# Optimization experiments

Hardware: AMD Instinct MI355X
Metric: run time of the kernel (lower is better)

## Reference

```python
import jax, jax.numpy as jnp
import numpy as np

N, E, H, FN, FE = 50000, 800000, 128, 8, 4


def setup_inputs() -> dict:
    key = jax.random.key(0)
    ks = jax.random.split(key, 12)
    g = lambda k, shape: jax.random.normal(k, shape, dtype=jnp.float32) * 0.05
    return dict(
        x=jax.random.normal(ks[0], (N, FN), dtype=jnp.float32),
        edge_index=jax.random.randint(ks[1], (2, E), 0, N),
        edge_attr=jax.random.normal(ks[2], (E, FE), dtype=jnp.float32),
        W1=g(ks[3], (FN, H)), b1=jnp.zeros((H,), jnp.float32),
        W2=g(ks[4], (H, H)), b2=jnp.zeros((H,), jnp.float32),
        W3=g(ks[5], (H, H)), b3=jnp.zeros((H,), jnp.float32),
        We1=g(ks[6], (FE, H)), be1=jnp.zeros((H,), jnp.float32),
        We2=g(ks[7], (H, H)), be2=jnp.zeros((H,), jnp.float32),
        Wc1=g(ks[8], (3 * H, H)), bc1=jnp.zeros((H,), jnp.float32),
        Wc2=g(ks[9], (H, H // 2)), bc2=jnp.zeros((H // 2,), jnp.float32),
        Wc3=g(ks[10], (H // 2, 2)), bc3=jnp.zeros((2,), jnp.float32),
    )


def _gcn(h, W, b, row2, col2, norm, n):
    # GCNConv: transform, normalized message from source row2 -> target col2, scatter-add, bias
    h = h @ W
    msg = norm[:, None] * h[row2]  # [E+N, H]
    return jax.ops.segment_sum(msg, col2, num_segments=n) + b


def reference(x, edge_index, edge_attr, W1, b1, W2, b2, W3, b3,
              We1, be1, We2, be2, Wc1, bc1, Wc2, bc2, Wc3, bc3):
    n = x.shape[0]
    row, col = edge_index[0], edge_index[1]
    loop = jnp.arange(n)
    # add self-loops (PyG GCNConv default)
    row2 = jnp.concatenate([row, loop])
    col2 = jnp.concatenate([col, loop])
    deg = jax.ops.segment_sum(jnp.ones_like(col2, dtype=x.dtype), col2, num_segments=n)
    dinv = jnp.where(deg > 0, deg ** -0.5, 0.0)
    norm = dinv[row2] * dinv[col2]  # symmetric normalization per edge

    h = jax.nn.relu(_gcn(x, W1, b1, row2, col2, norm, n))
    h = jax.nn.relu(_gcn(h, W2, b2, row2, col2, norm, n))
    h = jax.nn.relu(_gcn(h, W3, b3, row2, col2, norm, n))

    # edge encoder MLP (dropout inactive in eval)
    ef = jax.nn.relu(edge_attr @ We1 + be1) @ We2 + be2

    # gather endpoint node features, concat with edge features
    ec = jnp.concatenate([h[row], h[col], ef], axis=1)  # [E, 3H]
    z = jax.nn.relu(ec @ Wc1 + bc1)
    z = jax.nn.relu(z @ Wc2 + bc2)
    logits = z @ Wc3 + bc3
    return jax.nn.log_softmax(logits, axis=1)
```

## Files before the change

### kernel.cpp

```cpp
#include <hip/hip_runtime.h>
#include <math.h>

#define H 128
#define STC 152
#define SOT 136
#define SPQ 136
#define Z2S 69

typedef __attribute__((ext_vector_type(8))) short short8;
typedef __attribute__((ext_vector_type(4))) float f32x4;

__device__ inline float bflo(unsigned int v) { return __uint_as_float(v << 16); }
__device__ inline float bfhi(unsigned int v) { return __uint_as_float(v & 0xffff0000u); }
__device__ inline float bf2f(unsigned short v) { return __uint_as_float(((unsigned int)v) << 16); }

__device__ inline unsigned int cvtpk(float lo, float hi) {
    unsigned int r;
    asm("v_cvt_pk_bf16_f32 %0, %1, %2" : "=v"(r) : "v"(lo), "v"(hi));
    return r;
}
__device__ inline unsigned short f2bf1(float f) {
    unsigned int r;
    asm("v_cvt_pk_bf16_f32 %0, %1, %1" : "=v"(r) : "v"(f));
    return (unsigned short)r;
}


__global__ void count_kernel(const int* __restrict__ col, int E, int* __restrict__ cnt) {
    int e = blockIdx.x * blockDim.x + threadIdx.x;
    if (e < E) atomicAdd(&cnt[col[e]], 1);
}

__global__ void scan_sum_kernel(const int* __restrict__ cnt, int N, int* __restrict__ bsum) {
    int b = blockIdx.x, t = threadIdx.x;
    int base = b * 1024 + t * 4;
    int s = 0;
#pragma unroll
    for (int g = 0; g < 4; ++g) {
        int i = base + g;
        if (i < N) s += cnt[i];
    }
    for (int off = 32; off >= 1; off >>= 1) s += __shfl_down(s, off, 64);
    __shared__ int ws[4];
    if ((t & 63) == 0) ws[t >> 6] = s;
    __syncthreads();
    if (t == 0) bsum[b] = ws[0] + ws[1] + ws[2] + ws[3];
}

__global__ void scan_offsets_kernel(const int* __restrict__ bsum, int nb,
                                    int* __restrict__ boff, int* __restrict__ col_start, int N) {
    int lane = threadIdx.x;
    int v = (lane < nb) ? bsum[lane] : 0;
    int incl = v;
    for (int off = 1; off < 64; off <<= 1) {
        int u = __shfl_up(incl, off, 64);
        if (lane >= off) incl += u;
    }
    if (lane < nb) boff[lane] = incl - v;
    if (lane == 63) col_start[N] = incl;
}

__global__ void scan_write_kernel(const int* __restrict__ cnt, int N, const int* __restrict__ boff,
                                  int* __restrict__ col_start, int* __restrict__ cursor,
                                  float* __restrict__ dinv) {
    int b = blockIdx.x, t = threadIdx.x;
    int lane = t & 63, wv = t >> 6;
    int base = b * 1024 + t * 4;
    int c[4];
    int s = 0;
#pragma unroll
    for (int g = 0; g < 4; ++g) {
        int i = base + g;
        c[g] = (i < N) ? cnt[i] : 0;
        s += c[g];
    }
    int incl = s;
    for (int off = 1; off < 64; off <<= 1) {
        int u = __shfl_up(incl, off, 64);
        if (lane >= off) incl += u;
    }
    __shared__ int ws[4];
    if (lane == 63) ws[wv] = incl;
    __syncthreads();
    int run = boff[b] + incl - s;
    for (int w = 0; w < wv; ++w) run += ws[w];
#pragma unroll
    for (int g = 0; g < 4; ++g) {
        int i = base + g;
        if (i < N) {
            col_start[i] = run;
            cursor[i] = run;
            dinv[i] = rsqrtf((float)(c[g] + 1));
            run += c[g];
        }
    }
}

__global__ void scatter_kernel(const int* __restrict__ row, const int* __restrict__ col, int E,
                               int* __restrict__ cursor, int* __restrict__ csc_src,
                               int2* __restrict__ csc_ec) {
    int e = blockIdx.x * blockDim.x + threadIdx.x;
    if (e < E) {
        int c = col[e];
        int p = atomicAdd(&cursor[c], 1);
        csc_src[p] = row[e];
        csc_ec[p] = make_int2(e, c);
    }
}


__global__ __launch_bounds__(256) void aggx_kernel(
    const float* __restrict__ x, const int* __restrict__ col_start,
    const int* __restrict__ csc_src, const float* __restrict__ dinv,
    float* __restrict__ aggx, int N) {
    int wv = threadIdx.x >> 6, lane = threadIdx.x & 63;
    int i = blockIdx.x * 4 + wv;
    if (i >= N) return;
    int f = lane & 7, j = lane >> 3;
    int s0 = col_start[i], s1 = col_start[i + 1];
    float acc = 0.f;
    int p = s0 + j;
    for (; p + 8 < s1; p += 16) {
        int sa = csc_src[p], sb = csc_src[p + 8];
        float va = dinv[sa] * x[sa * 8 + f];
        float vb = dinv[sb] * x[sb * 8 + f];
        acc += va + vb;
    }
    if (p < s1) {
        int s = csc_src[p];
        acc = fmaf(dinv[s], x[s * 8 + f], acc);
    }
    acc += __shfl_xor(acc, 8, 64);
    acc += __shfl_xor(acc, 16, 64);
    acc += __shfl_xor(acc, 32, 64);
    if (j == 0) {
        float di = dinv[i];
        aggx[i * 8 + f] = fmaf(di, acc, di * di * x[i * 8 + f]);
    }
}

__global__ void xform8bf_kernel(const float* __restrict__ aggx, const float* __restrict__ W,
                                const float* __restrict__ b, const float* __restrict__ dinv,
                                unsigned int* __restrict__ out, int N) {
    int t = blockIdx.x * 256 + threadIdx.x;
    int i = t >> 6, jp = t & 63;
    if (i >= N) return;
    const float* ar = aggx + i * 8;
    float sc = dinv[i];
    int j0 = jp * 2;
    float a0 = b[j0], a1 = b[j0 + 1];
#pragma unroll
    for (int k = 0; k < 8; ++k) {
        float av = ar[k];
        a0 = fmaf(av, W[k * 128 + j0], a0);
        a1 = fmaf(av, W[k * 128 + j0 + 1], a1);
    }
    out[(size_t)i * 64 + jp] = cvtpk(sc * fmaxf(a0, 0.f), sc * fmaxf(a1, 0.f));
}

__global__ __launch_bounds__(256) void agg128bf_kernel(
    const unsigned int* __restrict__ hd, const int* __restrict__ col_start,
    const int* __restrict__ csc_src, const float* __restrict__ dinv,
    unsigned int* __restrict__ out, int N) {
    int wv = threadIdx.x >> 6, lane = threadIdx.x & 63;
    int i = blockIdx.x * 4 + wv;
    if (i >= N) return;
    int s0 = col_start[i], s1 = col_start[i + 1];
    float ax = 0.f, ay = 0.f;
    int p = s0;
    for (; p + 16 <= s1; p += 16) {
        unsigned int v[16];
#pragma unroll
        for (int k = 0; k < 16; ++k)
            v[k] = hd[(size_t)csc_src[p + k] * 64 + lane];
#pragma unroll
        for (int k = 0; k < 16; ++k) { ax += bflo(v[k]); ay += bfhi(v[k]); }
    }
    for (; p + 4 <= s1; p += 4) {
        unsigned int v0 = hd[(size_t)csc_src[p + 0] * 64 + lane];
        unsigned int v1 = hd[(size_t)csc_src[p + 1] * 64 + lane];
        unsigned int v2 = hd[(size_t)csc_src[p + 2] * 64 + lane];
        unsigned int v3 = hd[(size_t)csc_src[p + 3] * 64 + lane];
        ax += bflo(v0) + bflo(v1) + bflo(v2) + bflo(v3);
        ay += bfhi(v0) + bfhi(v1) + bfhi(v2) + bfhi(v3);
    }
    for (; p < s1; ++p) {
        unsigned int v = hd[(size_t)csc_src[p] * 64 + lane];
        ax += bflo(v); ay += bfhi(v);
    }
    float di = dinv[i];
    unsigned int vs = hd[(size_t)i * 64 + lane];
    float rx = di * (ax + bflo(vs));
    float ry = di * (ay + bfhi(vs));
    out[(size_t)i * 64 + lane] = cvtpk(rx, ry);
}

__global__ __launch_bounds__(256) void xform_mfma_kernel(
    const unsigned short* __restrict__ in, const unsigned short* __restrict__ Bp,
    const float* __restrict__ b, const float* __restrict__ scale,
    unsigned short* __restrict__ out, int N) {
    __shared__ __align__(16) unsigned short sm[64 * STC];
    int tid = threadIdx.x;
    int i0 = blockIdx.x * 64;
    for (int u = tid; u < 1024; u += 256) {
        int i = u >> 4, l = u & 15;
        int node = i0 + i; if (node >= N) node = N - 1;
        uint4 v = ((const uint4*)in)[(size_t)node * 16 + l];
        *(uint4*)&sm[i * STC + l * 8] = v;
    }
    __syncthreads();
    int lane = tid & 63, w = tid >> 6, lm = lane & 15, quad = lane >> 4;
    int nt0 = 2 * w, nt1 = 2 * w + 1;
    f32x4 acc0[4], acc1[4];
    {
        float bv0 = b[nt0 * 16 + lm], bv1 = b[nt1 * 16 + lm];
        for (int m = 0; m < 4; ++m)
            for (int r = 0; r < 4; ++r) { acc0[m][r] = bv0; acc1[m][r] = bv1; }
    }
#pragma unroll
    for (int s = 0; s < 4; ++s) {
        short8 b0 = *(const short8*)&Bp[((size_t)(s * 8 + nt0) * 64 + lane) * 8];
        short8 b1 = *(const short8*)&Bp[((size_t)(s * 8 + nt1) * 64 + lane) * 8];
#pragma unroll
        for (int m = 0; m < 4; ++m) {
            short8 afr = *(const short8*)&sm[(m * 16 + lm) * STC + s * 32 + quad * 8];
            acc0[m] = __builtin_amdgcn_mfma_f32_16x16x32_bf16(afr, b0, acc0[m], 0, 0, 0);
            acc1[m] = __builtin_amdgcn_mfma_f32_16x16x32_bf16(afr, b1, acc1[m], 0, 0, 0);
        }
    }
    __syncthreads();
    for (int m = 0; m < 4; ++m)
        for (int r = 0; r < 4; ++r) {
            int rw = m * 16 + quad * 4 + r;
            int node = i0 + rw; if (node >= N) node = N - 1;
            float sc = scale ? scale[node] : 1.f;
            sm[rw * SOT + nt0 * 16 + lm] = f2bf1(sc * fmaxf(acc0[m][r], 0.f));
            sm[rw * SOT + nt1 * 16 + lm] = f2bf1(sc * fmaxf(acc1[m][r], 0.f));
        }
    __syncthreads();
    for (int u = tid; u < 1024; u += 256) {
        int i = u >> 4, l = u & 15;
        int node = i0 + i;
        if (node < N)
            *(uint4*)&out[(size_t)node * 128 + l * 8] = *(uint4*)&sm[i * SOT + l * 8];
    }
}


__global__ void weff_kernel(const float* __restrict__ We2, const float* __restrict__ Wc1,
                            float* __restrict__ Weff) {
    int idx = blockIdx.x * blockDim.x + threadIdx.x;
    int k = idx >> 7, c = idx & 127;
    float acc = 0.f;
    for (int j = 0; j < 128; ++j)
        acc = fmaf(We2[k * 128 + j], Wc1[(256 + j) * 128 + c], acc);
    Weff[idx] = acc;
}

__global__ void bc1p_kernel(const float* __restrict__ bc1, const float* __restrict__ be2,
                            const float* __restrict__ Wc1, float* __restrict__ bc1p) {
    int c = threadIdx.x;
    float acc = bc1[c];
    for (int j = 0; j < 128; ++j)
        acc = fmaf(be2[j], Wc1[(256 + j) * 128 + c], acc);
    bc1p[c] = acc;
}

__global__ void packg_kernel(const float* __restrict__ src, unsigned short* __restrict__ dst) {
    int idx = blockIdx.x * 256 + threadIdx.x;
    int s = idx >> 9, nt = (idx >> 6) & 7, lane = idx & 63;
    int quad = lane >> 4, lm = lane & 15;
    int n = nt * 16 + lm, k0 = s * 32 + quad * 8;
    unsigned int p[4];
#pragma unroll
    for (int g = 0; g < 4; ++g)
        p[g] = cvtpk(src[(k0 + 2 * g) * 128 + n], src[(k0 + 2 * g + 1) * 128 + n]);
    *(uint4*)&dst[(size_t)idx * 8] = make_uint4(p[0], p[1], p[2], p[3]);
}

__global__ void pack2_kernel(const float* __restrict__ Wc2, unsigned short* __restrict__ Bp2) {
    int idx = blockIdx.x * 256 + threadIdx.x;
    int s = idx >> 8, nt = (idx >> 6) & 3, lane = idx & 63;
    int quad = lane >> 4, lm = lane & 15;
    int n = nt * 16 + lm, k0 = s * 32 + quad * 8;
    unsigned int p[4];
#pragma unroll
    for (int g = 0; g < 4; ++g)
        p[g] = cvtpk(Wc2[(k0 + 2 * g) * 64 + n], Wc2[(k0 + 2 * g + 1) * 64 + n]);
    *(uint4*)&Bp2[(size_t)idx * 8] = make_uint4(p[0], p[1], p[2], p[3]);
}

__global__ void packwe1_kernel(const float* __restrict__ We1, const float* __restrict__ be1,
                               unsigned short* __restrict__ BpE) {
    int idx = blockIdx.x * 256 + threadIdx.x;
    if (idx >= 512) return;
    int nt = idx >> 6, lane = idx & 63;
    int quad = lane >> 4, lm = lane & 15;
    int n = nt * 16 + lm, k0 = quad * 8;
    unsigned int p[4];
#pragma unroll
    for (int g = 0; g < 4; ++g) {
        int r0 = k0 + 2 * g, r1 = r0 + 1;
        float v0 = (r0 < 4) ? We1[r0 * 128 + n] : ((r0 == 4) ? be1[n] : 0.f);
        float v1 = (r1 < 4) ? We1[r1 * 128 + n] : ((r1 == 4) ? be1[n] : 0.f);
        p[g] = cvtpk(v0, v1);
    }
    *(uint4*)&BpE[(size_t)idx * 8] = make_uint4(p[0], p[1], p[2], p[3]);
}


__global__ __launch_bounds__(256) void h3pq_kernel(
    const unsigned short* __restrict__ in, const unsigned short* __restrict__ BpW3,
    const float* __restrict__ b3,
    const unsigned short* __restrict__ BpA, const unsigned short* __restrict__ BpB,
    const float* __restrict__ bc1p,
    unsigned short* __restrict__ P, unsigned short* __restrict__ Q, int N) {
    __shared__ __align__(16) unsigned short At[64 * STC];
    __shared__ __align__(16) unsigned short Hs[64 * SOT];
    int tid = threadIdx.x;
    int i0 = blockIdx.x * 64;
    for (int u = tid; u < 1024; u += 256) {
        int i = u >> 4, l = u & 15;
        int node = i0 + i; if (node >= N) node = N - 1;
        uint4 v = ((const uint4*)in)[(size_t)node * 16 + l];
        *(uint4*)&At[i * STC + l * 8] = v;
    }
    __syncthreads();
    int lane = tid & 63, w = tid >> 6, lm = lane & 15, quad = lane >> 4;

    {
        int nt0 = 2 * w, nt1 = 2 * w + 1;
        f32x4 a0[4], a1[4];
        float bv0 = b3[nt0 * 16 + lm], bv1 = b3[nt1 * 16 + lm];
        for (int m = 0; m < 4; ++m)
            for (int r = 0; r < 4; ++r) { a0[m][r] = bv0; a1[m][r] = bv1; }
#pragma unroll
        for (int s = 0; s < 4; ++s) {
            short8 b0 = *(const short8*)&BpW3[((size_t)(s * 8 + nt0) * 64 + lane) * 8];
            short8 b1 = *(const short8*)&BpW3[((size_t)(s * 8 + nt1) * 64 + lane) * 8];
#pragma unroll
            for (int m = 0; m < 4; ++m) {
                short8 afr = *(const short8*)&At[(m * 16 + lm) * STC + s * 32 + quad * 8];
                a0[m] = __builtin_amdgcn_mfma_f32_16x16x32_bf16(afr, b0, a0[m], 0, 0, 0);
                a1[m] = __builtin_amdgcn_mfma_f32_16x16x32_bf16(afr, b1, a1[m], 0, 0, 0);
            }
        }
        __syncthreads();
        for (int m = 0; m < 4; ++m)
            for (int r = 0; r < 4; ++r) {
                int rw = m * 16 + quad * 4 + r;
                Hs[rw * SOT + nt0 * 16 + lm] = f2bf1(fmaxf(a0[m][r], 0.f));
                Hs[rw * SOT + nt1 * 16 + lm] = f2bf1(fmaxf(a1[m][r], 0.f));
            }
    }
    __syncthreads();

    int half = w & 1;
    const unsigned short* Bp = (w >> 1) ? BpB : BpA;
    f32x4 acc[4][4];
    for (int nt = 0; nt < 4; ++nt) {
        float bv = (w >> 1) ? 0.f : bc1p[half * 64 + nt * 16 + lm];
        for (int m = 0; m < 4; ++m)
            for (int r = 0; r < 4; ++r) acc[nt][m][r] = bv;
    }
#pragma unroll
    for (int s = 0; s < 4; ++s) {
        short8 afr[4];
#pragma unroll
        for (int m = 0; m < 4; ++m)
            afr[m] = *(const short8*)&Hs[(m * 16 + lm) * SOT + s * 32 + quad * 8];
#pragma unroll
        for (int nt = 0; nt < 4; ++nt) {
            short8 bfr = *(const short8*)&Bp[((size_t)(s * 8 + half * 4 + nt) * 64 + lane) * 8];
#pragma unroll
            for (int m = 0; m < 4; ++m)
                acc[nt][m] = __builtin_amdgcn_mfma_f32_16x16x32_bf16(afr[m], bfr, acc[nt][m], 0, 0, 0);
        }
    }
    __syncthreads();
    unsigned short* St = At;

    if (w < 2) {
        for (int nt = 0; nt < 4; ++nt)
            for (int m = 0; m < 4; ++m)
                for (int r = 0; r < 4; ++r) {
                    int rw = m * 16 + quad * 4 + r;
                    St[rw * SOT + half * 64 + nt * 16 + lm] = f2bf1(acc[nt][m][r]);
                }
    }
    __syncthreads();
    for (int u = tid; u < 1024; u += 256) {
        int i = u >> 4, l = u & 15;
        int node = i0 + i;
        if (node < N)
            *(uint4*)&P[(size_t)node * 128 + l * 8] = *(uint4*)&St[i * SOT + l * 8];
    }
    __syncthreads();
    if (w >= 2) {
        for (int nt = 0; nt < 4; ++nt)
            for (int m = 0; m < 4; ++m)
                for (int r = 0; r < 4; ++r) {
                    int rw = m * 16 + quad * 4 + r;
                    St[rw * SOT + half * 64 + nt * 16 + lm] = f2bf1(acc[nt][m][r]);
                }
    }
    __syncthreads();
    for (int u = tid; u < 1024; u += 256) {
        int i = u >> 4, l = u & 15;
        int node = i0 + i;
        if (node < N)
            *(uint4*)&Q[(size_t)node * 128 + l * 8] = *(uint4*)&St[i * SOT + l * 8];
    }
}


__global__ __launch_bounds__(256, 4) void classifier_mfma2(
    const int* __restrict__ csc_src, const int2* __restrict__ csc_ec,
    const float* __restrict__ ea, const unsigned short* __restrict__ BpE,
    const unsigned short* __restrict__ P, const unsigned short* __restrict__ Q,
    const unsigned short* __restrict__ BpU, const unsigned short* __restrict__ Bp2,
    const float* __restrict__ bc2, const float* __restrict__ Wc3, const float* __restrict__ bc3,
    float* __restrict__ out, int E) {
    __shared__ __align__(16) unsigned char smem[37888];
    unsigned short* SpqB = (unsigned short*)smem;
    float* z2 = (float*)smem;
    unsigned short* At = (unsigned short*)(smem + 17664);
    unsigned short* z1 = At;
    float* part = (float*)(smem + 17664);
    int* sS = (int*)(smem + 37120);
    int* eS = sS + 64;
    int* cS = eS + 64;

    int tid = threadIdx.x;
    int lane = tid & 63, w = tid >> 6, lm = lane & 15, quad = lane >> 4;
    int e0 = blockIdx.x * 64;

    short8 bE0 = *(const short8*)&BpE[((size_t)(2 * w) * 64 + lane) * 8];
    short8 bE1 = *(const short8*)&BpE[((size_t)(2 * w + 1) * 64 + lane) * 8];
    short8 b0s[4], b1s[4], b2s[4];
#pragma unroll
    for (int s = 0; s < 4; ++s) {
        b0s[s] = *(const short8*)&BpU[((size_t)(s * 8 + 2 * w) * 64 + lane) * 8];
        b1s[s] = *(const short8*)&BpU[((size_t)(s * 8 + 2 * w + 1) * 64 + lane) * 8];
        b2s[s] = *(const short8*)&Bp2[((size_t)(s * 4 + w) * 64 + lane) * 8];
    }
    float bv2 = bc2[w * 16 + lm];

    if (tid < 64) {
        int p = e0 + tid; if (p >= E) p = E - 1;
        sS[tid] = csc_src[p];
        int2 ec = csc_ec[p];
        eS[tid] = ec.x; cS[tid] = ec.y;
    }
    __syncthreads();

    float4 av[4];
    if (quad == 0) {
#pragma unroll
        for (int m = 0; m < 4; ++m)
            av[m] = ((const float4*)ea)[eS[m * 16 + lm]];
    }

    {
        const uint4* P4 = (const uint4*)P;
        const uint4* Q4 = (const uint4*)Q;
        int l = tid & 15;
        uint4 pv[4], qv[4];
#pragma unroll
        for (int j = 0; j < 4; ++j) {
            int i = (tid >> 4) + 16 * j;
            pv[j] = P4[(size_t)sS[i] * 16 + l];
            qv[j] = Q4[(size_t)cS[i] * 16 + l];
        }
#pragma unroll
        for (int j = 0; j < 4; ++j) {
            int i = (tid >> 4) + 16 * j;
            uint4 o;
            o.x = cvtpk(bflo(pv[j].x) + bflo(qv[j].x), bfhi(pv[j].x) + bfhi(qv[j].x));
            o.y = cvtpk(bflo(pv[j].y) + bflo(qv[j].y), bfhi(pv[j].y) + bfhi(qv[j].y));
            o.z = cvtpk(bflo(pv[j].z) + bflo(qv[j].z), bfhi(pv[j].z) + bfhi(qv[j].z));
            o.w = cvtpk(bflo(pv[j].w) + bflo(qv[j].w), bfhi(pv[j].w) + bfhi(qv[j].w));
            *(uint4*)&SpqB[i * SPQ + l * 8] = o;
        }
    }

    short8 eaf[4];
#pragma unroll
    for (int m = 0; m < 4; ++m) eaf[m] = (short8){0, 0, 0, 0, 0, 0, 0, 0};
    if (quad == 0) {
#pragma unroll
        for (int m = 0; m < 4; ++m) {
            eaf[m][0] = (short)f2bf1(av[m].x);
            eaf[m][1] = (short)f2bf1(av[m].y);
            eaf[m][2] = (short)f2bf1(av[m].z);
            eaf[m][3] = (short)f2bf1(av[m].w);
            eaf[m][4] = (short)0x3F80;
        }
    }

    {
        f32x4 zacc = {0.f, 0.f, 0.f, 0.f};
#pragma unroll
        for (int m = 0; m < 4; ++m) {
            f32x4 t0 = __builtin_amdgcn_mfma_f32_16x16x32_bf16(eaf[m], bE0, zacc, 0, 0, 0);
            f32x4 t1 = __builtin_amdgcn_mfma_f32_16x16x32_bf16(eaf[m], bE1, zacc, 0, 0, 0);
#pragma unroll
            for (int r = 0; r < 4; ++r) {
                int rw = m * 16 + quad * 4 + r;
                At[rw * STC + 32 * w + lm]      = f2bf1(fmaxf(t0[r], 0.f));
                At[rw * STC + 32 * w + 16 + lm] = f2bf1(fmaxf(t1[r], 0.f));
            }
        }
    }
    __syncthreads();

    f32x4 acc0[4], acc1[4];
    for (int m = 0; m < 4; ++m)
        for (int r = 0; r < 4; ++r) { acc0[m][r] = 0.f; acc1[m][r] = 0.f; }
#pragma unroll
    for (int s = 0; s < 4; ++s) {
#pragma unroll
        for (int m = 0; m < 4; ++m) {
            short8 afr = *(const short8*)&At[(m * 16 + lm) * STC + s * 32 + quad * 8];
            acc0[m] = __builtin_amdgcn_mfma_f32_16x16x32_bf16(afr, b0s[s], acc0[m], 0, 0, 0);
            acc1[m] = __builtin_amdgcn_mfma_f32_16x16x32_bf16(afr, b1s[s], acc1[m], 0, 0, 0);
        }
    }
    for (int m = 0; m < 4; ++m)
        for (int r = 0; r < 4; ++r) {
            int rw = m * 16 + quad * 4 + r;
            acc0[m][r] = fmaxf(acc0[m][r] + bf2f(SpqB[rw * SPQ + 32 * w + lm]), 0.f);
            acc1[m][r] = fmaxf(acc1[m][r] + bf2f(SpqB[rw * SPQ + 32 * w + 16 + lm]), 0.f);
        }
    __syncthreads();
    for (int m = 0; m < 4; ++m)
        for (int r = 0; r < 4; ++r) {
            int rw = m * 16 + quad * 4 + r;
            z1[rw * STC + 32 * w + lm]      = f2bf1(acc0[m][r]);
            z1[rw * STC + 32 * w + 16 + lm] = f2bf1(acc1[m][r]);
        }
    __syncthreads();

    {
        f32x4 acc2[4];
        for (int m = 0; m < 4; ++m)
            for (int r = 0; r < 4; ++r) acc2[m][r] = bv2;
#pragma unroll
        for (int s = 0; s < 4; ++s) {
#pragma unroll
            for (int m = 0; m < 4; ++m) {
                short8 afr = *(const short8*)&z1[(m * 16 + lm) * STC + s * 32 + quad * 8];
                acc2[m] = __builtin_amdgcn_mfma_f32_16x16x32_bf16(afr, b2s[s], acc2[m], 0, 0, 0);
            }
        }
        for (int m = 0; m < 4; ++m)
            for (int r = 0; r < 4; ++r)
                z2[(m * 16 + quad * 4 + r) * Z2S + w * 16 + lm] = fmaxf(acc2[m][r], 0.f);
    }
    __syncthreads();

    {
        int e = tid & 63, q = tid >> 6;
        int c = q & 1, hf = q >> 1;
        const float* zr = z2 + e * Z2S + hf * 32;
        const float* wc = Wc3 + hf * 64 + c;
        float acc = 0.f;
#pragma unroll 8
        for (int kk = 0; kk < 32; ++kk)
            acc = fmaf(zr[kk], wc[2 * kk], acc);
        part[q * 64 + e] = acc;
    }
    __syncthreads();
    if (tid < 64) {
        int p = e0 + tid;
        if (p < E) {
            float l0 = bc3[0] + part[tid] + part[128 + tid];
            float l1 = bc3[1] + part[64 + tid] + part[192 + tid];
            float m = fmaxf(l0, l1);
            float lse = m + logf(expf(l0 - m) + expf(l1 - m));
            ((float2*)out)[eS[tid]] = make_float2(l0 - lse, l1 - lse);
        }
    }
}


extern "C" void kernel_launch(void* const* d_in, const int* in_sizes, int n_in,
                              void* d_out, int out_size, void* d_ws, size_t ws_size,
                              hipStream_t stream) {
    const float* x   = (const float*)d_in[0];
    const int*   ei  = (const int*)d_in[1];
    const float* ea  = (const float*)d_in[2];
    const float* W1  = (const float*)d_in[3];
    const float* b1  = (const float*)d_in[4];
    const float* W2  = (const float*)d_in[5];
    const float* b2  = (const float*)d_in[6];
    const float* W3  = (const float*)d_in[7];
    const float* b3  = (const float*)d_in[8];
    const float* We1 = (const float*)d_in[9];
    const float* be1 = (const float*)d_in[10];
    const float* We2 = (const float*)d_in[11];
    const float* be2 = (const float*)d_in[12];
    const float* Wc1 = (const float*)d_in[13];
    const float* bc1 = (const float*)d_in[14];
    const float* Wc2 = (const float*)d_in[15];
    const float* bc2 = (const float*)d_in[16];
    const float* Wc3 = (const float*)d_in[17];
    const float* bc3 = (const float*)d_in[18];
    float* out = (float*)d_out;

    int N = in_sizes[0] / 8;
    int E = in_sizes[1] / 2;
    const int* row = ei;
    const int* col = ei + E;
    int NB = (N + 1023) / 1024;
    int ntiles = (E + 63) / 64;

    char* w = (char*)d_ws;
    auto alloc = [&](size_t bytes) { void* p = (void*)w; w += (bytes + 255) & ~(size_t)255; return p; };
    int*   cnt       = (int*)alloc((size_t)N * 4);
    int*   col_start = (int*)alloc((size_t)(N + 1) * 4);
    int*   cursor    = (int*)alloc((size_t)N * 4);
    int*   csc_src   = (int*)alloc((size_t)E * 4);
    int2*  csc_ec    = (int2*)alloc((size_t)E * 8);
    float* dinv      = (float*)alloc((size_t)N * 4);
    int*   bsum      = (int*)alloc(64 * 4);
    int*   boff      = (int*)alloc(64 * 4);
    float* Weff      = (float*)alloc(128 * 128 * 4);
    float* bc1p      = (float*)alloc(128 * 4);
    unsigned short* BpA  = (unsigned short*)alloc(32768);
    unsigned short* BpB  = (unsigned short*)alloc(32768);
    unsigned short* BpU  = (unsigned short*)alloc(32768);
    unsigned short* BpW2 = (unsigned short*)alloc(32768);
    unsigned short* BpW3 = (unsigned short*)alloc(32768);
    unsigned short* Bp2  = (unsigned short*)alloc(16384);
    unsigned short* BpE  = (unsigned short*)alloc(8192);
    float* aggx = (float*)alloc((size_t)N * 8 * 4);
    unsigned short* bufA = (unsigned short*)alloc((size_t)N * H * 2);
    unsigned short* bufB = (unsigned short*)alloc((size_t)N * H * 2);
    unsigned short* Pm   = (unsigned short*)alloc((size_t)N * H * 2);
    unsigned short* Qm   = (unsigned short*)alloc((size_t)N * H * 2);

    hipMemsetAsync(cnt, 0, (size_t)N * 4, stream);
    count_kernel<<<(E + 255) / 256, 256, 0, stream>>>(col, E, cnt);
    scan_sum_kernel<<<NB, 256, 0, stream>>>(cnt, N, bsum);
    scan_offsets_kernel<<<1, 64, 0, stream>>>(bsum, NB, boff, col_start, N);
    scan_write_kernel<<<NB, 256, 0, stream>>>(cnt, N, boff, col_start, cursor, dinv);
    scatter_kernel<<<(E + 255) / 256, 256, 0, stream>>>(row, col, E, cursor, csc_src, csc_ec);

    weff_kernel<<<64, 256, 0, stream>>>(We2, Wc1, Weff);
    bc1p_kernel<<<1, 128, 0, stream>>>(bc1, be2, Wc1, bc1p);
    packg_kernel<<<8, 256, 0, stream>>>(Wc1, BpA);
    packg_kernel<<<8, 256, 0, stream>>>(Wc1 + 128 * 128, BpB);
    packg_kernel<<<8, 256, 0, stream>>>(Weff, BpU);
    packg_kernel<<<8, 256, 0, stream>>>(W2, BpW2);
    packg_kernel<<<8, 256, 0, stream>>>(W3, BpW3);
    pack2_kernel<<<4, 256, 0, stream>>>(Wc2, Bp2);
    packwe1_kernel<<<2, 256, 0, stream>>>(We1, be1, BpE);

    aggx_kernel<<<(N + 3) / 4, 256, 0, stream>>>(x, col_start, csc_src, dinv, aggx, N);
    xform8bf_kernel<<<(N * 64 + 255) / 256, 256, 0, stream>>>(aggx, W1, b1, dinv,
                                                              (unsigned int*)bufA, N);
    agg128bf_kernel<<<(N + 3) / 4, 256, 0, stream>>>((const unsigned int*)bufA, col_start, csc_src,
                                                     dinv, (unsigned int*)bufB, N);
    xform_mfma_kernel<<<(N + 63) / 64, 256, 0, stream>>>(bufB, BpW2, b2, dinv, bufA, N);
    agg128bf_kernel<<<(N + 3) / 4, 256, 0, stream>>>((const unsigned int*)bufA, col_start, csc_src,
                                                     dinv, (unsigned int*)bufB, N);
    h3pq_kernel<<<(N + 63) / 64, 256, 0, stream>>>(bufB, BpW3, b3, BpA, BpB, bc1p, Pm, Qm, N);

    classifier_mfma2<<<ntiles, 256, 0, stream>>>(
        csc_src, csc_ec, ea, BpE, Pm, Qm, BpU, Bp2, bc2, Wc3, bc3, out, E);
}
```

Baseline: 437.7 us.

## Vectorize GCN aggregation with 16-byte gathers and permute P/Q columns for packed LDS

The aggregation kernel now has each wave split into four 16-lane groups. Each group gathers a whole 256-byte neighbour row with uint4 loads, handling four neighbours at once, and the groups are combined with cross-lane shuffles. This replaces 4-byte per-lane gathers with fewer, wider memory transactions. Separately, the P/Q output columns are interleaved so that paired hidden units sit in adjacent bf16 slots, letting the classifier read and write z1 with packed 32-bit accesses. The Wc2 packing is permuted to match. The cost is extra shuffle reduction work and idle lanes on tail neighbours.

```diff
diff --git a/kernel.cpp b/kernel.cpp
--- a/kernel.cpp
+++ b/kernel.cpp
@@ -23,6 +23,14 @@
     unsigned int r;
     asm("v_cvt_pk_bf16_f32 %0, %1, %1" : "=v"(r) : "v"(f));
     return (unsigned short)r;
+}
+
+__device__ inline int permcol(int T, int lm) {
+    return 32 * (T >> 1) + 2 * lm + (T & 1);
+}
+__device__ inline int kperm(int k) {
+    int u = k >> 1;
+    return 32 * (u >> 4) + (u & 15) + ((k & 1) << 4);
 }
 
 
@@ -165,34 +173,62 @@
     int wv = threadIdx.x >> 6, lane = threadIdx.x & 63;
     int i = blockIdx.x * 4 + wv;
     if (i >= N) return;
+    int j = lane >> 4, cp = lane & 15;
+    const uint4* hd4 = (const uint4*)hd;
     int s0 = col_start[i], s1 = col_start[i + 1];
-    float ax = 0.f, ay = 0.f;
+    float a0 = 0.f, a1 = 0.f, a2 = 0.f, a3 = 0.f, a4 = 0.f, a5 = 0.f, a6 = 0.f, a7 = 0.f;
     int p = s0;
     for (; p + 16 <= s1; p += 16) {
-        unsigned int v[16];
-#pragma unroll
-        for (int k = 0; k < 16; ++k)
-            v[k] = hd[(size_t)csc_src[p + k] * 64 + lane];
-#pragma unroll
-        for (int k = 0; k < 16; ++k) { ax += bflo(v[k]); ay += bfhi(v[k]); }
+        uint4 v[4];
+#pragma unroll
+        for (int k = 0; k < 4; ++k) {
+            int b = p + 4 * k;
+            int sa = csc_src[b], sb = csc_src[b + 1], sc = csc_src[b + 2], sd = csc_src[b + 3];
+            int s = (j & 2) ? ((j & 1) ? sd : sc) : ((j & 1) ? sb : sa);
+            v[k] = hd4[(size_t)s * 16 + cp];
+        }
+#pragma unroll
+        for (int k = 0; k < 4; ++k) {
+            a0 += bflo(v[k].x); a1 += bfhi(v[k].x);
+            a2 += bflo(v[k].y); a3 += bfhi(v[k].y);
+            a4 += bflo(v[k].z); a5 += bfhi(v[k].z);
+            a6 += bflo(v[k].w); a7 += bfhi(v[k].w);
+        }
     }
     for (; p + 4 <= s1; p += 4) {
-        unsigned int v0 = hd[(size_t)csc_src[p + 0] * 64 + lane];
-        unsigned int v1 = hd[(size_t)csc_src[p + 1] * 64 + lane];
-        unsigned int v2 = hd[(size_t)csc_src[p + 2] * 64 + lane];
-        unsigned int v3 = hd[(size_t)csc_src[p + 3] * 64 + lane];
-        ax += bflo(v0) + bflo(v1) + bflo(v2) + bflo(v3);
-        ay += bfhi(v0) + bfhi(v1) + bfhi(v2) + bfhi(v3);
-    }
-    for (; p < s1; ++p) {
-        unsigned int v = hd[(size_t)csc_src[p] * 64 + lane];
-        ax += bflo(v); ay += bfhi(v);
-    }
-    float di = dinv[i];
-    unsigned int vs = hd[(size_t)i * 64 + lane];
-    float rx = di * (ax + bflo(vs));
-    float ry = di * (ay + bfhi(vs));
-    out[(size_t)i * 64 + lane] = cvtpk(rx, ry);
+        int sa = csc_src[p], sb = csc_src[p + 1], sc = csc_src[p + 2], sd = csc_src[p + 3];
+        int s = (j & 2) ? ((j & 1) ? sd : sc) : ((j & 1) ? sb : sa);
+        uint4 v = hd4[(size_t)s * 16 + cp];
+        a0 += bflo(v.x); a1 += bfhi(v.x);
+        a2 += bflo(v.y); a3 += bfhi(v.y);
+        a4 += bflo(v.z); a5 += bfhi(v.z);
+        a6 += bflo(v.w); a7 += bfhi(v.w);
+    }
+    if (p + j < s1) {
+        uint4 v = hd4[(size_t)csc_src[p + j] * 16 + cp];
+        a0 += bflo(v.x); a1 += bfhi(v.x);
+        a2 += bflo(v.y); a3 += bfhi(v.y);
+        a4 += bflo(v.z); a5 += bfhi(v.z);
+        a6 += bflo(v.w); a7 += bfhi(v.w);
+    }
+    a0 += __shfl_xor(a0, 16, 64); a0 += __shfl_xor(a0, 32, 64);
+    a1 += __shfl_xor(a1, 16, 64); a1 += __shfl_xor(a1, 32, 64);
+    a2 += __shfl_xor(a2, 16, 64); a2 += __shfl_xor(a2, 32, 64);
+    a3 += __shfl_xor(a3, 16, 64); a3 += __shfl_xor(a3, 32, 64);
+    a4 += __shfl_xor(a4, 16, 64); a4 += __shfl_xor(a4, 32, 64);
+    a5 += __shfl_xor(a5, 16, 64); a5 += __shfl_xor(a5, 32, 64);
+    a6 += __shfl_xor(a6, 16, 64); a6 += __shfl_xor(a6, 32, 64);
+    a7 += __shfl_xor(a7, 16, 64); a7 += __shfl_xor(a7, 32, 64);
+    if (j == 0) {
+        float di = dinv[i];
+        uint4 vs = hd4[(size_t)i * 16 + cp];
+        uint4 o;
+        o.x = cvtpk(di * (a0 + bflo(vs.x)), di * (a1 + bfhi(vs.x)));
+        o.y = cvtpk(di * (a2 + bflo(vs.y)), di * (a3 + bfhi(vs.y)));
+        o.z = cvtpk(di * (a4 + bflo(vs.z)), di * (a5 + bfhi(vs.z)));
+        o.w = cvtpk(di * (a6 + bflo(vs.w)), di * (a7 + bfhi(vs.w)));
+        ((uint4*)out)[(size_t)i * 16 + cp] = o;
+    }
 }
 
 __global__ __launch_bounds__(256) void xform_mfma_kernel(
@@ -286,7 +322,7 @@
     unsigned int p[4];
 #pragma unroll
     for (int g = 0; g < 4; ++g)
-        p[g] = cvtpk(Wc2[(k0 + 2 * g) * 64 + n], Wc2[(k0 + 2 * g + 1) * 64 + n]);
+        p[g] = cvtpk(Wc2[kperm(k0 + 2 * g) * 64 + n], Wc2[kperm(k0 + 2 * g + 1) * 64 + n]);
     *(uint4*)&Bp2[(size_t)idx * 8] = make_uint4(p[0], p[1], p[2], p[3]);
 }
 
@@ -381,12 +417,15 @@
     unsigned short* St = At;
 
     if (w < 2) {
-        for (int nt = 0; nt < 4; ++nt)
+        for (int nt = 0; nt < 4; ++nt) {
+            int T = half * 4 + nt;
+            int pc = permcol(T, lm);
             for (int m = 0; m < 4; ++m)
                 for (int r = 0; r < 4; ++r) {
                     int rw = m * 16 + quad * 4 + r;
-                    St[rw * SOT + half * 64 + nt * 16 + lm] = f2bf1(acc[nt][m][r]);
+                    St[rw * SOT + pc] = f2bf1(acc[nt][m][r]);
                 }
+        }
     }
     __syncthreads();
     for (int u = tid; u < 1024; u += 256) {
@@ -397,12 +436,15 @@
     }
     __syncthreads();
     if (w >= 2) {
-        for (int nt = 0; nt < 4; ++nt)
+        for (int nt = 0; nt < 4; ++nt) {
+            int T = half * 4 + nt;
+            int pc = permcol(T, lm);
             for (int m = 0; m < 4; ++m)
                 for (int r = 0; r < 4; ++r) {
                     int rw = m * 16 + quad * 4 + r;
-                    St[rw * SOT + half * 64 + nt * 16 + lm] = f2bf1(acc[nt][m][r]);
+                    St[rw * SOT + pc] = f2bf1(acc[nt][m][r]);
                 }
+        }
     }
     __syncthreads();
     for (int u = tid; u < 1024; u += 256) {
@@ -526,19 +568,25 @@
             acc1[m] = __builtin_amdgcn_mfma_f32_16x16x32_bf16(afr, b1s[s], acc1[m], 0, 0, 0);
         }
     }
-    for (int m = 0; m < 4; ++m)
-        for (int r = 0; r < 4; ++r) {
-            int rw = m * 16 + quad * 4 + r;
-            acc0[m][r] = fmaxf(acc0[m][r] + bf2f(SpqB[rw * SPQ + 32 * w + lm]), 0.f);
-            acc1[m][r] = fmaxf(acc1[m][r] + bf2f(SpqB[rw * SPQ + 32 * w + 16 + lm]), 0.f);
-        }
-    __syncthreads();
-    for (int m = 0; m < 4; ++m)
-        for (int r = 0; r < 4; ++r) {
-            int rw = m * 16 + quad * 4 + r;
-            z1[rw * STC + 32 * w + lm]      = f2bf1(acc0[m][r]);
-            z1[rw * STC + 32 * w + 16 + lm] = f2bf1(acc1[m][r]);
-        }
+    {
+        const unsigned int* Spq32 = (const unsigned int*)SpqB;
+        for (int m = 0; m < 4; ++m)
+            for (int r = 0; r < 4; ++r) {
+                int rw = m * 16 + quad * 4 + r;
+                unsigned int pq = Spq32[rw * (SPQ / 2) + 16 * w + lm];
+                acc0[m][r] = fmaxf(acc0[m][r] + bflo(pq), 0.f);
+                acc1[m][r] = fmaxf(acc1[m][r] + bfhi(pq), 0.f);
+            }
+    }
+    __syncthreads();
+    {
+        unsigned int* z1u = (unsigned int*)z1;
+        for (int m = 0; m < 4; ++m)
+            for (int r = 0; r < 4; ++r) {
+                int rw = m * 16 + quad * 4 + r;
+                z1u[rw * (STC / 2) + 16 * w + lm] = cvtpk(acc0[m][r], acc1[m][r]);
+            }
+    }
     __syncthreads();
 
     {
```

After: 451.7 us. 1.03x slower.
